# Optimization experiments

Hardware: AMD Instinct MI355X
Metric: run time of the kernel (lower is better)

## Reference

```python
import jax, jax.numpy as jnp
import numpy as np

B, S, D, H, O, E, TOPK = 4, 2048, 512, 1024, 512, 8, 2


def setup_inputs() -> dict:
    key = jax.random.key(0)
    ks = jax.random.split(key, 6)
    s = lambda d: 1.0 / np.sqrt(d)
    return {
        "x": jax.random.normal(ks[0], (B, S, D), dtype=jnp.float32),
        "Wg": jax.random.normal(ks[1], (D, E), dtype=jnp.float32) * s(D),
        "W1": jax.random.normal(ks[2], (E, D, H), dtype=jnp.float32) * s(D),
        "b1": jnp.zeros((E, H), dtype=jnp.float32),
        "W2": jax.random.normal(ks[3], (E, H, O), dtype=jnp.float32) * s(H),
        "b2": jnp.zeros((E, O), dtype=jnp.float32),
    }


def reference(x, Wg, W1, b1, W2, b2):
    Bsz, Seq, Din = x.shape
    T = Bsz * Seq
    xm = x.reshape(T, Din)                       # [T, D] token matrix
    # router: softmax over experts, then top-k (ProbabilitySamplerTopk)
    probs = jax.nn.softmax(xm @ Wg, axis=-1)     # [T, E]
    top_p, top_i = jax.lax.top_k(probs, TOPK)    # [T, k]
    # dense scattered gates (topKProbabilitiesScattered in _computeGating);
    # zero entries for non-selected experts make the einsum combine exactly
    # equal to the original gather->per-expert-GEMM->index_add pipeline.
    gates = jnp.zeros((T, E), dtype=probs.dtype).at[
        jnp.arange(T)[:, None], top_i
    ].set(top_p)                                 # [T, E]
    # per-expert 2-layer MLP (inputExperts -> activation -> outputExperts)
    h = jax.nn.gelu(jnp.einsum("td,edh->teh", xm, W1) + b1[None])  # [T, E, H]
    y = jnp.einsum("teh,eho->teo", h, W2) + b2[None]               # [T, E, O]
    # weighted combine (multiply_by_gates + index_add)
    out = jnp.einsum("te,teo->to", gates, y)     # [T, O]
    return out.reshape(Bsz, Seq, O)
```

## Files before the change

kernel.cpp:

```cpp
#include <hip/hip_runtime.h>

#define T_TOK 8192
#define DIM   512
#define HID   1024
#define OUTD  512
#define NE    8

typedef __attribute__((ext_vector_type(8))) short short8v;
typedef __attribute__((ext_vector_type(4))) float f32x4;

__device__ __forceinline__ unsigned short f2bf(float f) {
  unsigned int u = __builtin_bit_cast(unsigned int, f);
  u += 0x7fffu + ((u >> 16) & 1u);
  return (unsigned short)(u >> 16);
}

__device__ __forceinline__ void gload_lds16(const void* g, void* l) {
  __builtin_amdgcn_global_load_lds(
      (__attribute__((address_space(1))) void*)g,
      (__attribute__((address_space(3))) void*)l, 16, 0, 0);
}

__device__ __forceinline__ float gelu_f(float v) {
  const float c0 = 0.7978845608028654f;
  float u = c0 * (v + 0.044715f * v * v * v);
  return 0.5f * v * (1.0f + tanhf(u));
}

__global__ __launch_bounds__(256) void k_transpose_cvt(
    const float* __restrict__ in, unsigned short* __restrict__ outp, int R, int C) {
  __shared__ float tile[32][33];
  int e = blockIdx.z;
  const float* inE = in + (size_t)e * R * C;
  unsigned short* outE = outp + (size_t)e * R * C;
  int c0 = blockIdx.x * 32, r0 = blockIdx.y * 32;
  int x = threadIdx.x, y = threadIdx.y;
#pragma unroll
  for (int i = 0; i < 32; i += 8)
    tile[y + i][x] = inE[(size_t)(r0 + y + i) * C + (c0 + x)];
  __syncthreads();
#pragma unroll
  for (int i = 0; i < 32; i += 8)
    outE[(size_t)(c0 + y + i) * R + (r0 + x)] = f2bf(tile[x][y + i]);
}

__global__ __launch_bounds__(256) void k_router(
    const float* __restrict__ x, const float* __restrict__ Wg,
    int* __restrict__ top_e, float* __restrict__ top_p) {
  int lane = threadIdx.x & 63;
  int t = blockIdx.x * 4 + (threadIdx.x >> 6);
  const float* xr = x + (size_t)t * DIM;
  int j0 = lane * 8;
  float4 xa = *(const float4*)(xr + j0);
  float4 xb = *(const float4*)(xr + j0 + 4);
  float xl[8] = {xa.x, xa.y, xa.z, xa.w, xb.x, xb.y, xb.z, xb.w};
  float acc[8] = {0.f,0.f,0.f,0.f,0.f,0.f,0.f,0.f};
#pragma unroll
  for (int jj = 0; jj < 8; ++jj) {
    float4 w0 = *(const float4*)(Wg + (size_t)(j0 + jj) * NE);
    float4 w1 = *(const float4*)(Wg + (size_t)(j0 + jj) * NE + 4);
    acc[0] += xl[jj] * w0.x; acc[1] += xl[jj] * w0.y;
    acc[2] += xl[jj] * w0.z; acc[3] += xl[jj] * w0.w;
    acc[4] += xl[jj] * w1.x; acc[5] += xl[jj] * w1.y;
    acc[6] += xl[jj] * w1.z; acc[7] += xl[jj] * w1.w;
  }
#pragma unroll
  for (int off = 32; off >= 1; off >>= 1) {
#pragma unroll
    for (int e2 = 0; e2 < 8; ++e2) acc[e2] += __shfl_xor(acc[e2], off, 64);
  }
  if (lane == 0) {
    float m = acc[0];
#pragma unroll
    for (int e2 = 1; e2 < 8; ++e2) m = fmaxf(m, acc[e2]);
    float p[8]; float s = 0.f;
#pragma unroll
    for (int e2 = 0; e2 < 8; ++e2) { p[e2] = expf(acc[e2] - m); s += p[e2]; }
    float inv = 1.f / s;
    int i0 = 0;
#pragma unroll
    for (int e2 = 1; e2 < 8; ++e2) if (p[e2] > p[i0]) i0 = e2;
    int i1 = (i0 == 0) ? 1 : 0;
#pragma unroll
    for (int e2 = 0; e2 < 8; ++e2) if (e2 != i0 && p[e2] > p[i1]) i1 = e2;
    top_e[t * 2] = i0;  top_e[t * 2 + 1] = i1;
    top_p[t * 2] = p[i0] * inv;  top_p[t * 2 + 1] = p[i1] * inv;
  }
}

__global__ __launch_bounds__(256) void k_plan(
    const int* __restrict__ top_e, int* __restrict__ localRank,
    int* __restrict__ blockCounts) {
  __shared__ int cnt[4][NE];
  __shared__ int wbase[4][NE];
  int tid = threadIdx.x, lane = tid & 63, w = tid >> 6;
  int a = blockIdx.x * 256 + tid;
  int e = top_e[a];
  int rank = 0;
#pragma unroll
  for (int e2 = 0; e2 < NE; ++e2) {
    unsigned long long m = __ballot(e == e2);
    if (e == e2) rank = __popcll(m & ((1ULL << lane) - 1ULL));
    if (lane == 0) cnt[w][e2] = __popcll(m);
  }
  __syncthreads();
  if (tid < NE) {
    int s = 0;
#pragma unroll
    for (int w2 = 0; w2 < 4; ++w2) { wbase[w2][tid] = s; s += cnt[w2][tid]; }
    blockCounts[blockIdx.x * NE + tid] = s;
  }
  __syncthreads();
  localRank[a] = wbase[w][e] + rank;
}

__global__ void k_scan2(const int* __restrict__ blockCounts, int* __restrict__ baseBlk,
                        int* __restrict__ offs, int nBlocks) {
  __shared__ int tot[NE];
  int tid = threadIdx.x;
  if (tid < NE) {
    int s = 0;
    for (int b = 0; b < nBlocks; ++b) { baseBlk[b * NE + tid] = s; s += blockCounts[b * NE + tid]; }
    tot[tid] = s;
  }
  __syncthreads();
  if (tid == 0) {
    int s = 0;
    for (int e = 0; e < NE; ++e) { offs[e] = s; s += tot[e]; }
    offs[NE] = s;
  }
}

__global__ __launch_bounds__(256) void k_scatter(
    const float* __restrict__ x, const int* __restrict__ top_e,
    const int* __restrict__ localRank, const int* __restrict__ baseBlk,
    const int* __restrict__ offs, int* __restrict__ pos_of,
    unsigned short* __restrict__ Xp) {
  int lane = threadIdx.x & 63;
  int a = blockIdx.x * 4 + (threadIdx.x >> 6);
  int t = a >> 1;
  int e = top_e[a];
  int pos = offs[e] + baseBlk[(a >> 8) * NE + e] + localRank[a];
  if (lane == 0) pos_of[a] = pos;
  const float* xr = x + (size_t)t * DIM + lane * 8;
  float4 xa = *(const float4*)xr;
  float4 xb = *(const float4*)(xr + 4);
  short8v pk;
  pk[0] = (short)f2bf(xa.x); pk[1] = (short)f2bf(xa.y);
  pk[2] = (short)f2bf(xa.z); pk[3] = (short)f2bf(xa.w);
  pk[4] = (short)f2bf(xb.x); pk[5] = (short)f2bf(xb.y);
  pk[6] = (short)f2bf(xb.z); pk[7] = (short)f2bf(xb.w);
  *(short8v*)(Xp + (size_t)pos * DIM + lane * 8) = pk;
}

template<int EPI>
__global__ __launch_bounds__(256, 2) void k_gemm_bt(
    const unsigned short* __restrict__ A,
    const unsigned short* __restrict__ Bt,
    const float* __restrict__ bias,
    const int* __restrict__ offs,
    unsigned short* __restrict__ Hout, float* __restrict__ Yout, int K, int N) {
  int e = blockIdx.z;
  int rowBeg = offs[e], rowEnd = offs[e + 1];
  int m0 = rowBeg + (int)blockIdx.y * 128;
  if (m0 >= rowEnd) return;
  int n0 = blockIdx.x * 128;
  const unsigned short* Be = Bt + (size_t)e * N * K;

  __shared__ __align__(16) unsigned short As[128 * 64];
  __shared__ __align__(16) unsigned short Bs[128 * 64];

  int tid = threadIdx.x, lane = tid & 63, w = tid >> 6;
  int wr = w >> 1, wc = w & 1;
  int rIn = lane >> 3;
  int cChunk = (lane & 7) * 8;
  int fr = lane & 15, fq = lane >> 4;

  f32x4 acc[4][4];
#pragma unroll
  for (int m = 0; m < 4; ++m)
#pragma unroll
    for (int n = 0; n < 4; ++n) acc[m][n] = (f32x4){0.f, 0.f, 0.f, 0.f};

  for (int k0 = 0; k0 < K; k0 += 64) {
#pragma unroll
    for (int t4 = 0; t4 < 4; ++t4) {
      int g = w * 4 + t4;
      int ar = m0 + g * 8 + rIn;
      if (ar > rowEnd - 1) ar = rowEnd - 1;
      gload_lds16(A + (size_t)ar * K + k0 + cChunk, &As[g * 8 * 64]);
      int br = n0 + g * 8 + rIn;
      gload_lds16(Be + (size_t)br * K + k0 + cChunk, &Bs[g * 8 * 64]);
    }
    __syncthreads();
#pragma unroll
    for (int kk = 0; kk < 64; kk += 32) {
      short8v av[4], bv[4];
#pragma unroll
      for (int m = 0; m < 4; ++m)
        av[m] = *(const short8v*)&As[(wr * 64 + m * 16 + fr) * 64 + kk + fq * 8];
#pragma unroll
      for (int n = 0; n < 4; ++n)
        bv[n] = *(const short8v*)&Bs[(wc * 64 + n * 16 + fr) * 64 + kk + fq * 8];
#pragma unroll
      for (int m = 0; m < 4; ++m)
#pragma unroll
        for (int n = 0; n < 4; ++n)
          acc[m][n] = __builtin_amdgcn_mfma_f32_16x16x32_bf16(av[m], bv[n], acc[m][n], 0, 0, 0);
    }
    __syncthreads();
  }

#pragma unroll
  for (int m = 0; m < 4; ++m) {
#pragma unroll
    for (int j = 0; j < 4; ++j) {
      int row = m0 + wr * 64 + m * 16 + fq * 4 + j;
      if (row >= rowEnd) continue;
#pragma unroll
      for (int n = 0; n < 4; ++n) {
        int col = n0 + wc * 64 + n * 16 + fr;
        float v = acc[m][n][j] + bias[(size_t)e * N + col];
        if (EPI == 0) {
          Hout[(size_t)row * N + col] = f2bf(gelu_f(v));
        } else {
          Yout[(size_t)row * N + col] = v;
        }
      }
    }
  }
}

__global__ __launch_bounds__(256) void k_combine(
    const float* __restrict__ Y, const int* __restrict__ pos_of,
    const float* __restrict__ top_p, float* __restrict__ out) {
  int lane = threadIdx.x & 63;
  int t = blockIdx.x * 4 + (threadIdx.x >> 6);
  int p0 = pos_of[t * 2], p1 = pos_of[t * 2 + 1];
  float g0 = top_p[t * 2], g1 = top_p[t * 2 + 1];
  const float4* y0 = (const float4*)(Y + (size_t)p0 * OUTD + lane * 8);
  const float4* y1 = (const float4*)(Y + (size_t)p1 * OUTD + lane * 8);
  float4* o = (float4*)(out + (size_t)t * OUTD + lane * 8);
  float4 a0 = y0[0], a1 = y0[1], c0 = y1[0], c1 = y1[1];
  float4 r0, r1;
  r0.x = g0 * a0.x + g1 * c0.x; r0.y = g0 * a0.y + g1 * c0.y;
  r0.z = g0 * a0.z + g1 * c0.z; r0.w = g0 * a0.w + g1 * c0.w;
  r1.x = g0 * a1.x + g1 * c1.x; r1.y = g0 * a1.y + g1 * c1.y;
  r1.z = g0 * a1.z + g1 * c1.z; r1.w = g0 * a1.w + g1 * c1.w;
  o[0] = r0; o[1] = r1;
}

extern "C" void kernel_launch(void* const* d_in, const int* in_sizes, int n_in,
                              void* d_out, int out_size, void* d_ws, size_t ws_size,
                              hipStream_t stream) {
  const float* x  = (const float*)d_in[0];
  const float* Wg = (const float*)d_in[1];
  const float* W1 = (const float*)d_in[2];
  const float* b1 = (const float*)d_in[3];
  const float* W2 = (const float*)d_in[4];
  const float* b2 = (const float*)d_in[5];
  float* out = (float*)d_out;

  char* p = (char*)d_ws;
  auto take = [&](size_t bytes) { char* r = p; p += (bytes + 255) & ~(size_t)255; return r; };
  unsigned short* W1t = (unsigned short*)take((size_t)NE * DIM * HID * 2);
  unsigned short* W2t = (unsigned short*)take((size_t)NE * HID * OUTD * 2);
  unsigned short* Xp  = (unsigned short*)take((size_t)2 * T_TOK * DIM * 2);
  unsigned short* Hb  = (unsigned short*)take((size_t)2 * T_TOK * HID * 2);
  float*          Yb  = (float*)take((size_t)2 * T_TOK * OUTD * 4);
  int* offs = (int*)take(4096);
  int*   top_e  = (int*)take((size_t)2 * T_TOK * 4);
  float* top_pv = (float*)take((size_t)2 * T_TOK * 4);
  int*   pos_of = (int*)take((size_t)2 * T_TOK * 4);
  int* localRank   = (int*)take((size_t)2 * T_TOK * 4);
  int* blockCounts = (int*)take((size_t)64 * NE * 4);
  int* baseBlk     = (int*)take((size_t)64 * NE * 4);

  const int PLAN_BLOCKS = (2 * T_TOK) / 256;

  k_transpose_cvt<<<dim3(HID / 32, DIM / 32, NE), dim3(32, 8), 0, stream>>>(W1, W1t, DIM, HID);
  k_transpose_cvt<<<dim3(OUTD / 32, HID / 32, NE), dim3(32, 8), 0, stream>>>(W2, W2t, HID, OUTD);
  k_router<<<T_TOK / 4, 256, 0, stream>>>(x, Wg, top_e, top_pv);
  k_plan<<<PLAN_BLOCKS, 256, 0, stream>>>(top_e, localRank, blockCounts);
  k_scan2<<<1, 64, 0, stream>>>(blockCounts, baseBlk, offs, PLAN_BLOCKS);
  k_scatter<<<(2 * T_TOK) / 4, 256, 0, stream>>>(x, top_e, localRank, baseBlk, offs, pos_of, Xp);
  k_gemm_bt<0><<<dim3(HID / 128, 64, NE), 256, 0, stream>>>(Xp, W1t, b1, offs, Hb, nullptr, DIM, HID);
  k_gemm_bt<1><<<dim3(OUTD / 128, 64, NE), 256, 0, stream>>>(Hb, W2t, b2, offs, nullptr, Yb, HID, OUTD);
  k_combine<<<T_TOK / 4, 256, 0, stream>>>(Yb, pos_of, top_pv, out);
}
```

Measured before the change: 154.1 us.

## Replace expert GEMMs with 8-wave double-buffered, swizzled, interleaved MFMA pipeline

Replaces the 128x128 single-buffered expert GEMM with a 256xBN tile kernel using 8 waves, double-buffered LDS, XOR-swizzled LDS layout, and staged loads of the next K tile interleaved with MFMA quadrants under explicit vmcnt waits and barriers. It aims to hide global-load latency, avoid LDS bank conflicts, and raise operand reuse per block. The larger M tile wastes more work on partially filled expert row ranges, and the grid of 64 row-blocks per expert is still launched, leaving many blocks that exit early.

```diff
diff --git a/kernel.cpp b/kernel.cpp
--- a/kernel.cpp
+++ b/kernel.cpp
@@ -153,82 +153,152 @@
   *(short8v*)(Xp + (size_t)pos * DIM + lane * 8) = pk;
 }
 
-template<int EPI>
-__global__ __launch_bounds__(256, 2) void k_gemm_bt(
+#define VMW(nimm) do { asm volatile("s_waitcnt vmcnt(" #nimm ")" ::: "memory"); \
+                       __builtin_amdgcn_sched_barrier(0); } while (0)
+#define MFMA1(d, a, b) d = __builtin_amdgcn_mfma_f32_16x16x32_bf16(a, b, d, 0, 0, 0)
+
+template<int BN, int EPI>
+__global__ __launch_bounds__(512, 2) void k_gemm8(
     const unsigned short* __restrict__ A,
     const unsigned short* __restrict__ Bt,
     const float* __restrict__ bias,
     const int* __restrict__ offs,
     unsigned short* __restrict__ Hout, float* __restrict__ Yout, int K, int N) {
-  int e = blockIdx.z;
-  int rowBeg = offs[e], rowEnd = offs[e + 1];
-  int m0 = rowBeg + (int)blockIdx.y * 128;
+  constexpr int NH = BN / 128;
+  constexpr int NF = 2 * NH;
+  constexpr int BCH = BN / 128;
+
+  __shared__ __align__(16) unsigned short Al[2][256 * 64];
+  __shared__ __align__(16) unsigned short Bl[2][BN * 64];
+
+  const int e = blockIdx.z;
+  const int rowBeg = offs[e], rowEnd = offs[e + 1];
+  const int m0 = rowBeg + (int)blockIdx.y * 256;
   if (m0 >= rowEnd) return;
-  int n0 = blockIdx.x * 128;
+  const int n0 = blockIdx.x * BN;
   const unsigned short* Be = Bt + (size_t)e * N * K;
 
-  __shared__ __align__(16) unsigned short As[128 * 64];
-  __shared__ __align__(16) unsigned short Bs[128 * 64];
-
-  int tid = threadIdx.x, lane = tid & 63, w = tid >> 6;
-  int wr = w >> 1, wc = w & 1;
-  int rIn = lane >> 3;
-  int cChunk = (lane & 7) * 8;
-  int fr = lane & 15, fq = lane >> 4;
-
-  f32x4 acc[4][4];
-#pragma unroll
-  for (int m = 0; m < 4; ++m)
-#pragma unroll
-    for (int n = 0; n < 4; ++n) acc[m][n] = (f32x4){0.f, 0.f, 0.f, 0.f};
-
-  for (int k0 = 0; k0 < K; k0 += 64) {
-#pragma unroll
-    for (int t4 = 0; t4 < 4; ++t4) {
-      int g = w * 4 + t4;
-      int ar = m0 + g * 8 + rIn;
-      if (ar > rowEnd - 1) ar = rowEnd - 1;
-      gload_lds16(A + (size_t)ar * K + k0 + cChunk, &As[g * 8 * 64]);
-      int br = n0 + g * 8 + rIn;
-      gload_lds16(Be + (size_t)br * K + k0 + cChunk, &Bs[g * 8 * 64]);
-    }
-    __syncthreads();
-#pragma unroll
-    for (int kk = 0; kk < 64; kk += 32) {
-      short8v av[4], bv[4];
-#pragma unroll
-      for (int m = 0; m < 4; ++m)
-        av[m] = *(const short8v*)&As[(wr * 64 + m * 16 + fr) * 64 + kk + fq * 8];
-#pragma unroll
-      for (int n = 0; n < 4; ++n)
-        bv[n] = *(const short8v*)&Bs[(wc * 64 + n * 16 + fr) * 64 + kk + fq * 8];
-#pragma unroll
-      for (int m = 0; m < 4; ++m)
-#pragma unroll
-        for (int n = 0; n < 4; ++n)
-          acc[m][n] = __builtin_amdgcn_mfma_f32_16x16x32_bf16(av[m], bv[n], acc[m][n], 0, 0, 0);
-    }
-    __syncthreads();
-  }
-
-#pragma unroll
-  for (int m = 0; m < 4; ++m) {
+  const int tid = threadIdx.x;
+  const int lane = tid & 63, w = tid >> 6;
+  const int waveM = w >> 2, waveN = w & 3;
+  const int fr = lane & 15, fq = lane >> 4;
+  const int sRow = tid >> 3;
+  const int sCe = ((((tid & 7) << 4) ^ ((sRow & 7) << 4)) >> 1);
+  const int NT = K >> 6;
+
+  f32x4 acc[8][NF];
+#pragma unroll
+  for (int m = 0; m < 8; ++m)
+#pragma unroll
+    for (int n = 0; n < NF; ++n) acc[m][n] = (f32x4){0.f, 0.f, 0.f, 0.f};
+  short8v Af[4][2], Bf0[NH][2], Bf1[NH][2];
+
+#define STAGE_A(pb2, c, tk) do {                                              \
+    int gr_ = m0 + (c) * 64 + sRow; if (gr_ > rowEnd - 1) gr_ = rowEnd - 1;   \
+    gload_lds16(A + (size_t)gr_ * K + ((tk) << 6) + sCe,                      \
+                (char*)&Al[pb2][0] + (c) * 8192 + (w << 10)); } while (0)
+
+#define STAGE_BH(pb2, h, tk) do {                                             \
+    _Pragma("unroll")                                                         \
+    for (int c_ = 0; c_ < BCH; ++c_) {                                        \
+      int idx_ = c_ * 64 + sRow;                                              \
+      int r_ = (BN == 256) ? (n0 + (idx_ >> 5) * 64 + (h) * 32 + (idx_ & 31)) \
+                           : (n0 + (idx_ >> 4) * 32 + (h) * 16 + (idx_ & 15));\
+      gload_lds16(Be + (size_t)r_ * K + ((tk) << 6) + sCe,                    \
+                  (char*)&Bl[pb2][0] + (h) * (BN / 2) * 128 + c_ * 8192 + (w << 10)); \
+    } } while (0)
+
+#define LDA(pb2, h) do {                                                      \
+    _Pragma("unroll")                                                         \
+    for (int m_ = 0; m_ < 4; ++m_)                                            \
+      _Pragma("unroll")                                                       \
+      for (int kb_ = 0; kb_ < 2; ++kb_) {                                     \
+        int row_ = waveM * 128 + (h) * 64 + m_ * 16 + fr;                     \
+        int off_ = row_ * 128 + (((kb_ << 6) + (fq << 4)) ^ ((fr & 7) << 4)); \
+        Af[m_][kb_] = *(const short8v*)((const char*)&Al[pb2][0] + off_);     \
+      } } while (0)
+
+#define LDB(pb2, h, BF) do {                                                  \
+    _Pragma("unroll")                                                         \
+    for (int n_ = 0; n_ < NH; ++n_)                                           \
+      _Pragma("unroll")                                                       \
+      for (int kb_ = 0; kb_ < 2; ++kb_) {                                     \
+        int idx_ = waveN * (BN / 8) + n_ * 16 + fr;                           \
+        int off_ = (h) * (BN / 2) * 128 + idx_ * 128 +                        \
+                   (((kb_ << 6) + (fq << 4)) ^ ((fr & 7) << 4));              \
+        BF[n_][kb_] = *(const short8v*)((const char*)&Bl[pb2][0] + off_);     \
+      } } while (0)
+
+#define QUAD(h, bh, BF) do {                                                  \
+    __builtin_amdgcn_s_setprio(1);                                            \
+    _Pragma("unroll")                                                         \
+    for (int m_ = 0; m_ < 4; ++m_)                                            \
+      _Pragma("unroll")                                                       \
+      for (int n_ = 0; n_ < NH; ++n_) {                                       \
+        MFMA1(acc[(h) * 4 + m_][(bh) * NH + n_], Af[m_][0], BF[n_][0]);       \
+        MFMA1(acc[(h) * 4 + m_][(bh) * NH + n_], Af[m_][1], BF[n_][1]);       \
+      }                                                                       \
+    __builtin_amdgcn_s_setprio(0); } while (0)
+
+  STAGE_A(0, 0, 0); STAGE_A(0, 2, 0);
+  STAGE_BH(0, 0, 0);
+  STAGE_BH(0, 1, 0);
+  STAGE_A(0, 1, 0); STAGE_A(0, 3, 0);
+  if (BN == 256) VMW(4); else VMW(3);
+  __builtin_amdgcn_s_barrier();
+
+  for (int t = 0; t < NT; ++t) {
+    const int pb = t & 1, pn = pb ^ 1;
+    const bool nl = (t + 1 < NT);
+    LDA(pb, 0);
+    LDB(pb, 0, Bf0);
+    if (nl) { STAGE_A(pn, 0, t + 1); STAGE_A(pn, 2, t + 1); }
+    if (nl) VMW(4); else VMW(2);
+    __builtin_amdgcn_s_barrier();
+    QUAD(0, 0, Bf0);
+    __builtin_amdgcn_s_barrier();
+    LDB(pb, 1, Bf1);
+    if (nl) STAGE_BH(pn, 0, t + 1);
+    if (nl) { if (BN == 256) VMW(4); else VMW(3); } else VMW(0);
+    __builtin_amdgcn_s_barrier();
+    QUAD(0, 1, Bf1);
+    __builtin_amdgcn_s_barrier();
+    LDA(pb, 1);
+    if (nl) STAGE_BH(pn, 1, t + 1);
+    __builtin_amdgcn_s_barrier();
+    QUAD(1, 1, Bf1);
+    __builtin_amdgcn_s_barrier();
+    if (nl) { STAGE_A(pn, 1, t + 1); STAGE_A(pn, 3, t + 1); }
+    if (nl) { if (BN == 256) VMW(4); else VMW(3); }
+    __builtin_amdgcn_s_barrier();
+    QUAD(1, 0, Bf0);
+    __builtin_amdgcn_s_barrier();
+  }
+
+  float bv[NF];
+#pragma unroll
+  for (int nf = 0; nf < NF; ++nf)
+    bv[nf] = bias[(size_t)e * N + n0 + waveN * (BN / 4) + nf * 16 + fr];
+#pragma unroll
+  for (int mf = 0; mf < 8; ++mf) {
 #pragma unroll
     for (int j = 0; j < 4; ++j) {
-      int row = m0 + wr * 64 + m * 16 + fq * 4 + j;
+      int row = m0 + waveM * 128 + mf * 16 + fq * 4 + j;
       if (row >= rowEnd) continue;
 #pragma unroll
-      for (int n = 0; n < 4; ++n) {
-        int col = n0 + wc * 64 + n * 16 + fr;
-        float v = acc[m][n][j] + bias[(size_t)e * N + col];
-        if (EPI == 0) {
-          Hout[(size_t)row * N + col] = f2bf(gelu_f(v));
-        } else {
-          Yout[(size_t)row * N + col] = v;
-        }
+      for (int nf = 0; nf < NF; ++nf) {
+        int col = n0 + waveN * (BN / 4) + nf * 16 + fr;
+        float v = acc[mf][nf][j] + bv[nf];
+        if (EPI == 0) Hout[(size_t)row * N + col] = f2bf(gelu_f(v));
+        else          Yout[(size_t)row * N + col] = v;
       }
     }
   }
+#undef STAGE_A
+#undef STAGE_BH
+#undef LDA
+#undef LDB
+#undef QUAD
 }
 
 __global__ __launch_bounds__(256) void k_combine(
@@ -284,7 +354,7 @@
   k_plan<<<PLAN_BLOCKS, 256, 0, stream>>>(top_e, localRank, blockCounts);
   k_scan2<<<1, 64, 0, stream>>>(blockCounts, baseBlk, offs, PLAN_BLOCKS);
   k_scatter<<<(2 * T_TOK) / 4, 256, 0, stream>>>(x, top_e, localRank, baseBlk, offs, pos_of, Xp);
-  k_gemm_bt<0><<<dim3(HID / 128, 64, NE), 256, 0, stream>>>(Xp, W1t, b1, offs, Hb, nullptr, DIM, HID);
-  k_gemm_bt<1><<<dim3(OUTD / 128, 64, NE), 256, 0, stream>>>(Hb, W2t, b2, offs, nullptr, Yb, HID, OUTD);
+  k_gemm8<256, 0><<<dim3(HID / 256, 64, NE), 512, 0, stream>>>(Xp, W1t, b1, offs, Hb, nullptr, DIM, HID);
+  k_gemm8<128, 1><<<dim3(OUTD / 128, 64, NE), 512, 0, stream>>>(Hb, W2t, b2, offs, nullptr, Yb, HID, OUTD);
   k_combine<<<T_TOK / 4, 256, 0, stream>>>(Yb, pos_of, top_pv, out);
 }
```

Result: slower. 184.3 us (+19.6%).

## Double-buffer grouped GEMM LDS with swizzle and persistent row-tile loop

Applied to the files above, without the earlier changes.

Rewrites the grouped expert GEMM so it double-buffers A/B tiles in LDS. The next K-slice's global-to-LDS loads are issued while MFMAs run on the current one, with explicit vmcnt waits and barriers. It adds an XOR swizzle on LDS columns to avoid bank conflicts, raises MFMA priority with setprio, and uses a flattened 1D grid with a fixed y-grid that loops over row tiles. Together these replace the old grid, which launched 64 row-tiles per expert and exited most blocks early. The cost is twice the LDS per block, which may limit occupancy, and a hand-tuned wait count that must match the number of issued loads.

```diff
diff --git a/kernel.cpp b/kernel.cpp
--- a/kernel.cpp
+++ b/kernel.cpp
@@ -5,6 +5,7 @@
 #define HID   1024
 #define OUTD  512
 #define NE    8
+#define NYGRID 32
 
 typedef __attribute__((ext_vector_type(8))) short short8v;
 typedef __attribute__((ext_vector_type(4))) float f32x4;
@@ -153,82 +154,114 @@
   *(short8v*)(Xp + (size_t)pos * DIM + lane * 8) = pk;
 }
 
-template<int EPI>
-__global__ __launch_bounds__(256, 2) void k_gemm_bt(
+#define VMW(nimm) do { asm volatile("s_waitcnt vmcnt(" #nimm ")" ::: "memory"); \
+                       __builtin_amdgcn_sched_barrier(0); } while (0)
+#define MFMA1(d, a, b) d = __builtin_amdgcn_mfma_f32_16x16x32_bf16(a, b, d, 0, 0, 0)
+
+template<int NX, int EPI>
+__global__ __launch_bounds__(256, 2) void k_gemm_s(
     const unsigned short* __restrict__ A,
     const unsigned short* __restrict__ Bt,
     const float* __restrict__ bias,
     const int* __restrict__ offs,
     unsigned short* __restrict__ Hout, float* __restrict__ Yout, int K, int N) {
-  int e = blockIdx.z;
-  int rowBeg = offs[e], rowEnd = offs[e + 1];
-  int m0 = rowBeg + (int)blockIdx.y * 128;
-  if (m0 >= rowEnd) return;
-  int n0 = blockIdx.x * 128;
+  __shared__ __align__(16) unsigned short Al[2][128 * 64];
+  __shared__ __align__(16) unsigned short Bl[2][128 * 64];
+
+  const int bid = blockIdx.x;
+  const int e = bid & 7;
+  const int rem = bid >> 3;
+  const int x = rem % NX;
+  const int ybase = rem / NX;
+  const int rowBeg = offs[e], rowEnd = offs[e + 1];
+  const int n0 = x * 128;
   const unsigned short* Be = Bt + (size_t)e * N * K;
 
-  __shared__ __align__(16) unsigned short As[128 * 64];
-  __shared__ __align__(16) unsigned short Bs[128 * 64];
-
-  int tid = threadIdx.x, lane = tid & 63, w = tid >> 6;
-  int wr = w >> 1, wc = w & 1;
-  int rIn = lane >> 3;
-  int cChunk = (lane & 7) * 8;
-  int fr = lane & 15, fq = lane >> 4;
-
-  f32x4 acc[4][4];
-#pragma unroll
-  for (int m = 0; m < 4; ++m)
-#pragma unroll
-    for (int n = 0; n < 4; ++n) acc[m][n] = (f32x4){0.f, 0.f, 0.f, 0.f};
-
-  for (int k0 = 0; k0 < K; k0 += 64) {
-#pragma unroll
-    for (int t4 = 0; t4 < 4; ++t4) {
-      int g = w * 4 + t4;
-      int ar = m0 + g * 8 + rIn;
-      if (ar > rowEnd - 1) ar = rowEnd - 1;
-      gload_lds16(A + (size_t)ar * K + k0 + cChunk, &As[g * 8 * 64]);
-      int br = n0 + g * 8 + rIn;
-      gload_lds16(Be + (size_t)br * K + k0 + cChunk, &Bs[g * 8 * 64]);
+  const int tid = threadIdx.x, lane = tid & 63, w = tid >> 6;
+  const int wr = w >> 1, wc = w & 1;
+  const int fr = lane & 15, fq = lane >> 4;
+  const int sRow = tid >> 3;
+  const int sCe = ((((tid & 7) << 4) ^ ((sRow & 7) << 4)) >> 1);
+  const int NT = K >> 6;
+
+#define STAGE(pb2, tk) do {                                                   \
+    _Pragma("unroll")                                                         \
+    for (int c_ = 0; c_ < 4; ++c_) {                                          \
+      int ar_ = m0 + c_ * 32 + sRow; if (ar_ > rowEnd - 1) ar_ = rowEnd - 1;  \
+      gload_lds16(A + (size_t)ar_ * K + ((tk) << 6) + sCe,                    \
+                  (char*)&Al[pb2][0] + c_ * 4096 + (w << 10));                \
+    }                                                                         \
+    _Pragma("unroll")                                                         \
+    for (int c_ = 0; c_ < 4; ++c_) {                                          \
+      int br_ = n0 + c_ * 32 + sRow;                                          \
+      gload_lds16(Be + (size_t)br_ * K + ((tk) << 6) + sCe,                   \
+                  (char*)&Bl[pb2][0] + c_ * 4096 + (w << 10));                \
+    } } while (0)
+
+#define COMPUTE(pb2) do {                                                     \
+    _Pragma("unroll")                                                         \
+    for (int kk_ = 0; kk_ < 2; ++kk_) {                                       \
+      short8v av[4], bv[4];                                                   \
+      _Pragma("unroll")                                                       \
+      for (int m_ = 0; m_ < 4; ++m_) {                                        \
+        int row_ = wr * 64 + m_ * 16 + fr;                                    \
+        av[m_] = *(const short8v*)((const char*)&Al[pb2][0] + row_ * 128 +    \
+                   (((kk_ << 6) + (fq << 4)) ^ ((fr & 7) << 4)));             \
+      }                                                                       \
+      _Pragma("unroll")                                                       \
+      for (int n_ = 0; n_ < 4; ++n_) {                                        \
+        int row_ = wc * 64 + n_ * 16 + fr;                                    \
+        bv[n_] = *(const short8v*)((const char*)&Bl[pb2][0] + row_ * 128 +    \
+                   (((kk_ << 6) + (fq << 4)) ^ ((fr & 7) << 4)));             \
+      }                                                                       \
+      __builtin_amdgcn_s_setprio(1);                                          \
+      _Pragma("unroll")                                                       \
+      for (int m_ = 0; m_ < 4; ++m_)                                          \
+        _Pragma("unroll")                                                     \
+        for (int n_ = 0; n_ < 4; ++n_)                                        \
+          MFMA1(acc[m_][n_], av[m_], bv[n_]);                                 \
+      __builtin_amdgcn_s_setprio(0);                                          \
+    } } while (0)
+
+  for (int y = ybase; ; y += NYGRID) {
+    const int m0 = rowBeg + y * 128;
+    if (m0 >= rowEnd) break;
+
+    f32x4 acc[4][4];
+#pragma unroll
+    for (int m = 0; m < 4; ++m)
+#pragma unroll
+      for (int n = 0; n < 4; ++n) acc[m][n] = (f32x4){0.f, 0.f, 0.f, 0.f};
+
+    STAGE(0, 0);
+    STAGE(1, 1);
+    for (int t = 0; t < NT; ++t) {
+      const int pb = t & 1;
+      if (t + 1 < NT) VMW(8); else VMW(0);
+      __builtin_amdgcn_s_barrier();
+      COMPUTE(pb);
+      __builtin_amdgcn_s_barrier();
+      if (t + 2 < NT) STAGE(pb, t + 2);
     }
-    __syncthreads();
-#pragma unroll
-    for (int kk = 0; kk < 64; kk += 32) {
-      short8v av[4], bv[4];
-#pragma unroll
-      for (int m = 0; m < 4; ++m)
-        av[m] = *(const short8v*)&As[(wr * 64 + m * 16 + fr) * 64 + kk + fq * 8];
-#pragma unroll
-      for (int n = 0; n < 4; ++n)
-        bv[n] = *(const short8v*)&Bs[(wc * 64 + n * 16 + fr) * 64 + kk + fq * 8];
-#pragma unroll
-      for (int m = 0; m < 4; ++m)
-#pragma unroll
-        for (int n = 0; n < 4; ++n)
-          acc[m][n] = __builtin_amdgcn_mfma_f32_16x16x32_bf16(av[m], bv[n], acc[m][n], 0, 0, 0);
-    }
-    __syncthreads();
-  }
-
-#pragma unroll
-  for (int m = 0; m < 4; ++m) {
-#pragma unroll
-    for (int j = 0; j < 4; ++j) {
-      int row = m0 + wr * 64 + m * 16 + fq * 4 + j;
-      if (row >= rowEnd) continue;
-#pragma unroll
-      for (int n = 0; n < 4; ++n) {
-        int col = n0 + wc * 64 + n * 16 + fr;
-        float v = acc[m][n][j] + bias[(size_t)e * N + col];
-        if (EPI == 0) {
-          Hout[(size_t)row * N + col] = f2bf(gelu_f(v));
-        } else {
-          Yout[(size_t)row * N + col] = v;
+
+#pragma unroll
+    for (int m = 0; m < 4; ++m) {
+#pragma unroll
+      for (int j = 0; j < 4; ++j) {
+        int row = m0 + wr * 64 + m * 16 + fq * 4 + j;
+        if (row >= rowEnd) continue;
+#pragma unroll
+        for (int n = 0; n < 4; ++n) {
+          int col = n0 + wc * 64 + n * 16 + fr;
+          float v = acc[m][n][j] + bias[(size_t)e * N + col];
+          if (EPI == 0) Hout[(size_t)row * N + col] = f2bf(gelu_f(v));
+          else          Yout[(size_t)row * N + col] = v;
         }
       }
     }
   }
+#undef STAGE
+#undef COMPUTE
 }
 
 __global__ __launch_bounds__(256) void k_combine(
@@ -284,7 +317,7 @@
   k_plan<<<PLAN_BLOCKS, 256, 0, stream>>>(top_e, localRank, blockCounts);
   k_scan2<<<1, 64, 0, stream>>>(blockCounts, baseBlk, offs, PLAN_BLOCKS);
   k_scatter<<<(2 * T_TOK) / 4, 256, 0, stream>>>(x, top_e, localRank, baseBlk, offs, pos_of, Xp);
-  k_gemm_bt<0><<<dim3(HID / 128, 64, NE), 256, 0, stream>>>(Xp, W1t, b1, offs, Hb, nullptr, DIM, HID);
-  k_gemm_bt<1><<<dim3(OUTD / 128, 64, NE), 256, 0, stream>>>(Hb, W2t, b2, offs, nullptr, Yb, HID, OUTD);
+  k_gemm_s<8, 0><<<NE * 8 * NYGRID, 256, 0, stream>>>(Xp, W1t, b1, offs, Hb, nullptr, DIM, HID);
+  k_gemm_s<4, 1><<<NE * 4 * NYGRID, 256, 0, stream>>>(Hb, W2t, b2, offs, nullptr, Yb, HID, OUTD);
   k_combine<<<T_TOK / 4, 256, 0, stream>>>(Yb, pos_of, top_pv, out);
 }
```

New measurement: 168.1 us. 1.09x slower.

## Use compacted tile list with persistent grid and XOR-swizzled LDS in expert GEMMs

Applied to the files above, without the earlier changes.

The scan kernel now builds a compact list of (expert, row-start) tiles, so the grouped GEMMs no longer launch 64×8 y/z blocks of which most exit immediately. The GEMMs become grid-stride persistent loops over that tile list. The LDS layout is XOR-swizzled to cut bank conflicts on the MFMA operand reads. Launch bounds are raised to 4 waves per SIMD for occupancy. The tile arrays are capped at 256 entries, and the single-block scan now does a bit more serial work.

```diff
diff --git a/kernel.cpp b/kernel.cpp
--- a/kernel.cpp
+++ b/kernel.cpp
@@ -115,8 +115,11 @@
 }
 
 __global__ void k_scan2(const int* __restrict__ blockCounts, int* __restrict__ baseBlk,
-                        int* __restrict__ offs, int nBlocks) {
+                        int* __restrict__ offs, int* __restrict__ tileE,
+                        int* __restrict__ tileM0, int* __restrict__ nYTp, int nBlocks) {
   __shared__ int tot[NE];
+  __shared__ int ytb[NE + 1];
+  __shared__ int obase[NE];
   int tid = threadIdx.x;
   if (tid < NE) {
     int s = 0;
@@ -125,9 +128,21 @@
   }
   __syncthreads();
   if (tid == 0) {
-    int s = 0;
-    for (int e = 0; e < NE; ++e) { offs[e] = s; s += tot[e]; }
-    offs[NE] = s;
+    int s = 0, yb = 0;
+    for (int e = 0; e < NE; ++e) {
+      offs[e] = s; obase[e] = s; ytb[e] = yb;
+      yb += (tot[e] + 127) >> 7;
+      s += tot[e];
+    }
+    offs[NE] = s; ytb[NE] = yb; nYTp[0] = yb;
+  }
+  __syncthreads();
+  for (int e = 0; e < NE; ++e) {
+    int nt = ytb[e + 1] - ytb[e];
+    for (int i = tid; i < nt; i += 64) {
+      tileE[ytb[e] + i]  = e;
+      tileM0[ytb[e] + i] = obase[e] + i * 128;
+    }
   }
 }
 
@@ -153,78 +168,93 @@
   *(short8v*)(Xp + (size_t)pos * DIM + lane * 8) = pk;
 }
 
-template<int EPI>
-__global__ __launch_bounds__(256, 2) void k_gemm_bt(
+#define MFMA1(d, a, b) d = __builtin_amdgcn_mfma_f32_16x16x32_bf16(a, b, d, 0, 0, 0)
+
+template<int NX, int LOG2NX, int EPI>
+__global__ __launch_bounds__(256, 4) void k_gemm_p(
     const unsigned short* __restrict__ A,
     const unsigned short* __restrict__ Bt,
     const float* __restrict__ bias,
     const int* __restrict__ offs,
+    const int* __restrict__ tileE, const int* __restrict__ tileM0,
+    const int* __restrict__ nYTp,
     unsigned short* __restrict__ Hout, float* __restrict__ Yout, int K, int N) {
-  int e = blockIdx.z;
-  int rowBeg = offs[e], rowEnd = offs[e + 1];
-  int m0 = rowBeg + (int)blockIdx.y * 128;
-  if (m0 >= rowEnd) return;
-  int n0 = blockIdx.x * 128;
-  const unsigned short* Be = Bt + (size_t)e * N * K;
-
-  __shared__ __align__(16) unsigned short As[128 * 64];
-  __shared__ __align__(16) unsigned short Bs[128 * 64];
-
-  int tid = threadIdx.x, lane = tid & 63, w = tid >> 6;
-  int wr = w >> 1, wc = w & 1;
-  int rIn = lane >> 3;
-  int cChunk = (lane & 7) * 8;
-  int fr = lane & 15, fq = lane >> 4;
-
-  f32x4 acc[4][4];
-#pragma unroll
-  for (int m = 0; m < 4; ++m)
-#pragma unroll
-    for (int n = 0; n < 4; ++n) acc[m][n] = (f32x4){0.f, 0.f, 0.f, 0.f};
-
-  for (int k0 = 0; k0 < K; k0 += 64) {
-#pragma unroll
-    for (int t4 = 0; t4 < 4; ++t4) {
-      int g = w * 4 + t4;
-      int ar = m0 + g * 8 + rIn;
-      if (ar > rowEnd - 1) ar = rowEnd - 1;
-      gload_lds16(A + (size_t)ar * K + k0 + cChunk, &As[g * 8 * 64]);
-      int br = n0 + g * 8 + rIn;
-      gload_lds16(Be + (size_t)br * K + k0 + cChunk, &Bs[g * 8 * 64]);
+  __shared__ __align__(16) unsigned short Al[128 * 64];
+  __shared__ __align__(16) unsigned short Bl[128 * 64];
+
+  const int tid = threadIdx.x, lane = tid & 63, w = tid >> 6;
+  const int wr = w >> 1, wc = w & 1;
+  const int fr = lane & 15, fq = lane >> 4;
+  const int sRow = tid >> 3;
+  const int sCe = ((((tid & 7) << 4) ^ ((sRow & 7) << 4)) >> 1);
+  const int NT = K >> 6;
+  const int nWork = nYTp[0] << LOG2NX;
+
+  for (int idx = blockIdx.x; idx < nWork; idx += gridDim.x) {
+    const int yt = idx >> LOG2NX;
+    const int xb = idx & (NX - 1);
+    const int e = tileE[yt];
+    const int m0 = tileM0[yt];
+    const int rowEnd = offs[e + 1];
+    const int n0 = xb * 128;
+    const unsigned short* Be = Bt + (size_t)e * N * K;
+
+    f32x4 acc[4][4];
+#pragma unroll
+    for (int m = 0; m < 4; ++m)
+#pragma unroll
+      for (int n = 0; n < 4; ++n) acc[m][n] = (f32x4){0.f, 0.f, 0.f, 0.f};
+
+    for (int t = 0; t < NT; ++t) {
+#pragma unroll
+      for (int c_ = 0; c_ < 4; ++c_) {
+        int ar_ = m0 + c_ * 32 + sRow; if (ar_ > rowEnd - 1) ar_ = rowEnd - 1;
+        gload_lds16(A + (size_t)ar_ * K + (t << 6) + sCe,
+                    (char*)&Al[0] + c_ * 4096 + (w << 10));
+      }
+#pragma unroll
+      for (int c_ = 0; c_ < 4; ++c_) {
+        int br_ = n0 + c_ * 32 + sRow;
+        gload_lds16(Be + (size_t)br_ * K + (t << 6) + sCe,
+                    (char*)&Bl[0] + c_ * 4096 + (w << 10));
+      }
+      __syncthreads();
+#pragma unroll
+      for (int kk = 0; kk < 2; ++kk) {
+        short8v av[4], bv[4];
+#pragma unroll
+        for (int m = 0; m < 4; ++m) {
+          int row_ = wr * 64 + m * 16 + fr;
+          av[m] = *(const short8v*)((const char*)&Al[0] + row_ * 128 +
+                    (((kk << 6) + (fq << 4)) ^ ((fr & 7) << 4)));
+        }
+#pragma unroll
+        for (int n = 0; n < 4; ++n) {
+          int row_ = wc * 64 + n * 16 + fr;
+          bv[n] = *(const short8v*)((const char*)&Bl[0] + row_ * 128 +
+                    (((kk << 6) + (fq << 4)) ^ ((fr & 7) << 4)));
+        }
+#pragma unroll
+        for (int m = 0; m < 4; ++m)
+#pragma unroll
+          for (int n = 0; n < 4; ++n)
+            MFMA1(acc[m][n], av[m], bv[n]);
+      }
+      __syncthreads();
     }
-    __syncthreads();
-#pragma unroll
-    for (int kk = 0; kk < 64; kk += 32) {
-      short8v av[4], bv[4];
-#pragma unroll
-      for (int m = 0; m < 4; ++m)
-        av[m] = *(const short8v*)&As[(wr * 64 + m * 16 + fr) * 64 + kk + fq * 8];
-#pragma unroll
-      for (int n = 0; n < 4; ++n)
-        bv[n] = *(const short8v*)&Bs[(wc * 64 + n * 16 + fr) * 64 + kk + fq * 8];
-#pragma unroll
-      for (int m = 0; m < 4; ++m)
-#pragma unroll
-        for (int n = 0; n < 4; ++n)
-          acc[m][n] = __builtin_amdgcn_mfma_f32_16x16x32_bf16(av[m], bv[n], acc[m][n], 0, 0, 0);
-    }
-    __syncthreads();
-  }
-
-#pragma unroll
-  for (int m = 0; m < 4; ++m) {
-#pragma unroll
-    for (int j = 0; j < 4; ++j) {
-      int row = m0 + wr * 64 + m * 16 + fq * 4 + j;
-      if (row >= rowEnd) continue;
-#pragma unroll
-      for (int n = 0; n < 4; ++n) {
-        int col = n0 + wc * 64 + n * 16 + fr;
-        float v = acc[m][n][j] + bias[(size_t)e * N + col];
-        if (EPI == 0) {
-          Hout[(size_t)row * N + col] = f2bf(gelu_f(v));
-        } else {
-          Yout[(size_t)row * N + col] = v;
+
+#pragma unroll
+    for (int m = 0; m < 4; ++m) {
+#pragma unroll
+      for (int j = 0; j < 4; ++j) {
+        int row = m0 + wr * 64 + m * 16 + fq * 4 + j;
+        if (row >= rowEnd) continue;
+#pragma unroll
+        for (int n = 0; n < 4; ++n) {
+          int col = n0 + wc * 64 + n * 16 + fr;
+          float v = acc[m][n][j] + bias[(size_t)e * N + col];
+          if (EPI == 0) Hout[(size_t)row * N + col] = f2bf(gelu_f(v));
+          else          Yout[(size_t)row * N + col] = v;
         }
       }
     }
@@ -268,7 +298,10 @@
   unsigned short* Xp  = (unsigned short*)take((size_t)2 * T_TOK * DIM * 2);
   unsigned short* Hb  = (unsigned short*)take((size_t)2 * T_TOK * HID * 2);
   float*          Yb  = (float*)take((size_t)2 * T_TOK * OUTD * 4);
-  int* offs = (int*)take(4096);
+  int* offs   = (int*)take(4096);
+  int* tileE  = (int*)take(256 * 4);
+  int* tileM0 = (int*)take(256 * 4);
+  int* nYTp   = (int*)take(256);
   int*   top_e  = (int*)take((size_t)2 * T_TOK * 4);
   float* top_pv = (float*)take((size_t)2 * T_TOK * 4);
   int*   pos_of = (int*)take((size_t)2 * T_TOK * 4);
@@ -282,9 +315,9 @@
   k_transpose_cvt<<<dim3(OUTD / 32, HID / 32, NE), dim3(32, 8), 0, stream>>>(W2, W2t, HID, OUTD);
   k_router<<<T_TOK / 4, 256, 0, stream>>>(x, Wg, top_e, top_pv);
   k_plan<<<PLAN_BLOCKS, 256, 0, stream>>>(top_e, localRank, blockCounts);
-  k_scan2<<<1, 64, 0, stream>>>(blockCounts, baseBlk, offs, PLAN_BLOCKS);
+  k_scan2<<<1, 64, 0, stream>>>(blockCounts, baseBlk, offs, tileE, tileM0, nYTp, PLAN_BLOCKS);
   k_scatter<<<(2 * T_TOK) / 4, 256, 0, stream>>>(x, top_e, localRank, baseBlk, offs, pos_of, Xp);
-  k_gemm_bt<0><<<dim3(HID / 128, 64, NE), 256, 0, stream>>>(Xp, W1t, b1, offs, Hb, nullptr, DIM, HID);
-  k_gemm_bt<1><<<dim3(OUTD / 128, 64, NE), 256, 0, stream>>>(Hb, W2t, b2, offs, nullptr, Yb, HID, OUTD);
+  k_gemm_p<8, 3, 0><<<1024, 256, 0, stream>>>(Xp, W1t, b1, offs, tileE, tileM0, nYTp, Hb, nullptr, DIM, HID);
+  k_gemm_p<4, 2, 1><<<512, 256, 0, stream>>>(Hb, W2t, b2, offs, tileE, tileM0, nYTp, nullptr, Yb, HID, OUTD);
   k_combine<<<T_TOK / 4, 256, 0, stream>>>(Yb, pos_of, top_pv, out);
 }
```

Measured after the change: 158.8 us. 1.03x slower.
